# Performance work log

Hardware: AMD Instinct MI355X
Metric: run time of the kernel (lower is better)

## Reference

```python
import jax, jax.numpy as jnp
import numpy as np

BN_EPS = 1e-5


def setup_inputs() -> dict:
    key = jax.random.key(0)
    k1, k2, k3, k4 = jax.random.split(key, 4)
    B, H, W, C = 2, 256, 256, 256
    x = jax.random.normal(k1, (B, H, W, C), dtype=jnp.float32)
    # 1x1 conv weights (bias=False), randomly initialized each forward in the original
    w_down = jax.random.normal(k2, (16, C), dtype=jnp.float32) * (1.0 / np.sqrt(C))
    w_up = jax.random.normal(k3, (C, 16), dtype=jnp.float32) * (1.0 / np.sqrt(16))
    w_final = jax.random.normal(k4, (C, 2 * C), dtype=jnp.float32) * (1.0 / np.sqrt(2 * C))
    return {"x": x, "w_down": w_down, "w_up": w_up, "w_final": w_final}


def reference(x, w_down, w_up, w_final):
    # x: [B, H, W, C] -> NCHW
    x = jnp.transpose(x, (0, 3, 1, 2))  # [B, C, H, W]
    B, C, H, W = x.shape
    # fresh BatchNorm2d in training mode: batch stats, weight=1, bias=0
    mean = jnp.mean(x, axis=(0, 2, 3), keepdims=True)
    var = jnp.var(x, axis=(0, 2, 3), keepdims=True)  # biased variance
    xn = (x - mean) * jax.lax.rsqrt(var + BN_EPS)  # [B, C, H, W]
    # relu -> sigmoid
    a = jax.nn.sigmoid(jax.nn.relu(xn))
    # down-channel 1x1 conv: C -> 16
    y = jnp.einsum('oc,bchw->bohw', w_down, a)  # [B, 16, H, W]
    f = y.reshape(B, 16, H * W)  # flattened per-sample [16, HW]
    # channel self-attention; NOTE: source bug reuses Gram of sample 0 for sample 1
    G0 = f[0] @ f[0].T  # [16, 16]
    out0 = G0 @ f[0]    # [16, HW]
    out1 = G0 @ f[1]    # [16, HW]  (faithful to xcam4b = Dot(xcam3a, xcam1b))
    xcam4 = jnp.stack([out0, out1], axis=0).reshape(B, 16, H, W)
    # up-channel 1x1 conv: 16 -> C
    up = jnp.einsum('co,bohw->bchw', w_up, xcam4)  # [B, C, H, W]
    cat = jnp.concatenate([xn, up], axis=1)  # [B, 2C, H, W]
    # final down-channel 1x1 conv: 2C -> C
    out = jnp.einsum('oc,bchw->bohw', w_final, cat)  # [B, C, H, W]
    return out
```

## Files before the change

### kernel.cpp

```cpp
#include <hip/hip_runtime.h>
#include <hip/hip_bf16.h>
#include <stdint.h>

typedef __attribute__((ext_vector_type(8))) short bf16x8;
typedef __attribute__((ext_vector_type(4))) float f32x4;

#define CC 256
#define HWP 65536

__device__ __forceinline__ unsigned short f2bf(float f) {
    union { float f; unsigned int u; } v; v.f = f;
    unsigned int u = v.u;
    return (unsigned short)((u + 0x7fffu + ((u >> 16) & 1u)) >> 16);
}
__device__ __forceinline__ unsigned int pk2(float lo, float hi) {
    union { __hip_bfloat16 b; unsigned short s; } ul, uh;
    ul.b = __float2bfloat16(lo);
    uh.b = __float2bfloat16(hi);
    return (unsigned)ul.s | ((unsigned)uh.s << 16);
}
__device__ __forceinline__ float sigm_relu(float xn) {
    float xr = fmaxf(xn, 0.f);
    float e = __expf(-xr);
    return __builtin_amdgcn_rcpf(1.f + e);
}

__global__ __launch_bounds__(512, 8) void k1_part(const float* __restrict__ x,
                                                  float* __restrict__ part) {
    __shared__ float red[8][520];
    const int t = threadIdx.x, bid = blockIdx.x;
    const int c4 = (t & 63) * 4, po = t >> 6;
    const float* xp = x + ((size_t)(bid * 256 + po)) * CC + c4;
    f32x4 s = {0.f, 0.f, 0.f, 0.f}, q = {0.f, 0.f, 0.f, 0.f};
    #pragma unroll 8
    for (int p = 0; p < 32; ++p) {
        f32x4 v = *(const f32x4*)(xp + (size_t)p * 8 * CC);
        s += v; q += v * v;
    }
    *(f32x4*)&red[po][c4] = s;
    *(f32x4*)&red[po][256 + c4] = q;
    __syncthreads();
    float r = 0.f;
    #pragma unroll
    for (int po2 = 0; po2 < 8; ++po2) r += red[po2][t];
    part[bid * 512 + t] = r;
}

__global__ __launch_bounds__(256) void k2a_red(const float* __restrict__ part,
                                               float* __restrict__ p2) {
    int t = threadIdx.x, r = blockIdx.x;
    float s = 0.f, q = 0.f;
    #pragma unroll
    for (int i = 0; i < 16; ++i) {
        s += part[(size_t)(r * 16 + i) * 512 + t];
        q += part[(size_t)(r * 16 + i) * 512 + 256 + t];
    }
    p2[r * 512 + t] = s;
    p2[r * 512 + 256 + t] = q;
}

__global__ __launch_bounds__(256) void k2b_stats(const float* __restrict__ p2,
                                                 float* __restrict__ mg,
                                                 float* __restrict__ ig) {
    int c = threadIdx.x;
    float s = 0.f, q = 0.f;
    #pragma unroll
    for (int r = 0; r < 32; ++r) { s += p2[r * 512 + c]; q += p2[r * 512 + 256 + c]; }
    float mean = s * (1.f / 131072.f);
    float var  = q * (1.f / 131072.f) - mean * mean;
    mg[c] = mean;
    ig[c] = rsqrtf(var + 1e-5f);
}

__global__ __launch_bounds__(512) void k3_gram(const float* __restrict__ x,
                                               const float* __restrict__ wd,
                                               const float* __restrict__ mg,
                                               const float* __restrict__ ig,
                                               float* __restrict__ gpart) {
    __shared__ uint4 apack[2048];
    __shared__ float y_s[2][16][68];
    const int t = threadIdx.x;
    const int w = t >> 6, lm = t & 15, lk = (t >> 4) & 3;
    const int h = w & 1, ntile = w >> 1;
    uint4 wfrag[4];
    #pragma unroll
    for (int kt = 0; kt < 4; ++kt) {
        const int kbr = h * 16 + kt * 4 + lk;
        f32x4 wa = *(const f32x4*)(wd + lm * 256 + kbr * 8);
        f32x4 wb = *(const f32x4*)(wd + lm * 256 + kbr * 8 + 4);
        wfrag[kt] = (uint4){pk2(wa[0], wa[1]), pk2(wa[2], wa[3]),
                            pk2(wb[0], wb[1]), pk2(wb[2], wb[3])};
    }
    const int kb = t & 31, c0 = kb * 8, nb = t >> 5;
    f32x4 m0 = *(const f32x4*)(mg + c0), m1 = *(const f32x4*)(mg + c0 + 4);
    f32x4 i0 = *(const f32x4*)(ig + c0), i1 = *(const f32x4*)(ig + c0 + 4);
    const float mm[8] = {m0[0],m0[1],m0[2],m0[3],m1[0],m1[1],m1[2],m1[3]};
    const float ii[8] = {i0[0],i0[1],i0[2],i0[3],i1[0],i1[1],i1[2],i1[3]};
    const int o1 = t >> 4, o2 = t & 15;
    float g = 0.f;
    for (int st = 0; st < 4; ++st) {
        const float* xb = x + ((size_t)(blockIdx.x * 256 + st * 64 + nb)) * CC + c0;
        #pragma unroll
        for (int rep = 0; rep < 4; ++rep) {
            int n = rep * 16 + nb;
            const float* xp = xb + (size_t)rep * 16 * CC;
            f32x4 v0 = *(const f32x4*)xp;
            f32x4 v1 = *(const f32x4*)(xp + 4);
            float vv[8] = {v0[0],v0[1],v0[2],v0[3],v1[0],v1[1],v1[2],v1[3]};
            unsigned aw[4];
            #pragma unroll
            for (int hh = 0; hh < 4; ++hh) {
                float a0 = sigm_relu((vv[2*hh]   - mm[2*hh])   * ii[2*hh]);
                float a1 = sigm_relu((vv[2*hh+1] - mm[2*hh+1]) * ii[2*hh+1]);
                aw[hh] = pk2(a0, a1);
            }
            apack[kb * 64 + (n ^ kb)] = (uint4){aw[0], aw[1], aw[2], aw[3]};
        }
        __syncthreads();
        f32x4 accY = {0.f, 0.f, 0.f, 0.f};
        #pragma unroll
        for (int kt = 0; kt < 4; ++kt) {
            const int kbr = h * 16 + kt * 4 + lk;
            uint4 u = apack[kbr * 64 + ((ntile * 16 + lm) ^ kbr)];
            accY = __builtin_amdgcn_mfma_f32_16x16x32_bf16(*(bf16x8*)&wfrag[kt], *(bf16x8*)&u, accY, 0, 0, 0);
        }
        #pragma unroll
        for (int i = 0; i < 4; ++i) y_s[h][lk * 4 + i][ntile * 16 + lm] = accY[i];
        __syncthreads();
        if (t < 256) {
            #pragma unroll
            for (int p4 = 0; p4 < 16; ++p4) {
                f32x4 a0 = *(const f32x4*)&y_s[0][o1][p4 * 4];
                f32x4 a1 = *(const f32x4*)&y_s[1][o1][p4 * 4];
                f32x4 b0 = *(const f32x4*)&y_s[0][o2][p4 * 4];
                f32x4 b1 = *(const f32x4*)&y_s[1][o2][p4 * 4];
                f32x4 ya = a0 + a1, yb = b0 + b1;
                g += ya[0]*yb[0] + ya[1]*yb[1] + ya[2]*yb[2] + ya[3]*yb[3];
            }
        }
        __syncthreads();
    }
    if (t < 256) gpart[blockIdx.x * 256 + t] = g;
}

__global__ __launch_bounds__(256) void k45_wcb(const float* __restrict__ gpart,
                                               const float* __restrict__ wd,
                                               const float* __restrict__ wf,
                                               const float* __restrict__ wu,
                                               unsigned short* __restrict__ wcb) {
    __shared__ float G_s[256];
    __shared__ float R_s[16][256];
    __shared__ float M_s[16][17];
    const int t = threadIdx.x;
    float g = 0.f;
    #pragma unroll 8
    for (int i = 0; i < 256; ++i) g += gpart[i * 256 + t];
    G_s[t] = g;
    __syncthreads();
    #pragma unroll
    for (int o = 0; o < 16; ++o) {
        float r = 0.f;
        #pragma unroll
        for (int o2 = 0; o2 < 16; ++o2) r += G_s[o * 16 + o2] * wd[o2 * 256 + t];
        R_s[o][t] = r;
    }
    const int lr = t >> 4, j = t & 15;
    const int r = blockIdx.x * 16 + lr;
    const float* wfr = wf + (size_t)r * 512;
    float m = 0.f;
    for (int c = 0; c < 256; ++c) m += wfr[256 + c] * wu[c * 16 + j];
    M_s[lr][j] = m;
    __syncthreads();
    float Ml[16];
    #pragma unroll
    for (int o = 0; o < 16; ++o) Ml[o] = M_s[lr][o];
    unsigned short* wrow = wcb + (size_t)r * 512;
    for (int i = 0; i < 16; ++i) {
        int c = j + 16 * i;
        wrow[c] = f2bf(wfr[c]);
        float kv = 0.f;
        #pragma unroll
        for (int o = 0; o < 16; ++o) kv += Ml[o] * R_s[o][c];
        wrow[256 + c] = f2bf(kv);
    }
}

__global__ __launch_bounds__(512, 4) void k6_main(const float* __restrict__ x,
                                                  const unsigned short* __restrict__ wcb,
                                                  const float* __restrict__ mg,
                                                  const float* __restrict__ ig,
                                                  float* __restrict__ out) {
    __shared__ uint4 zpack[4096];
    const int t = threadIdx.x;
    const int tile = (blockIdx.x & 7) * 256 + (blockIdx.x >> 3);
    const int b = tile >> 10;
    const int pw = (tile & 1023) * 64;
    const int kb = t & 31, c0 = kb * 8, nb = t >> 5;
    f32x4 m0 = *(const f32x4*)(mg + c0), m1 = *(const f32x4*)(mg + c0 + 4);
    f32x4 i0 = *(const f32x4*)(ig + c0), i1 = *(const f32x4*)(ig + c0 + 4);
    const float mm[8] = {m0[0],m0[1],m0[2],m0[3],m1[0],m1[1],m1[2],m1[3]};
    const float ii[8] = {i0[0],i0[1],i0[2],i0[3],i1[0],i1[1],i1[2],i1[3]};
    const float* xb = x + ((size_t)(b * HWP + pw + nb)) * CC + c0;
    f32x4 v[8];
    #pragma unroll
    for (int rep = 0; rep < 4; ++rep) {
        v[2 * rep]     = *(const f32x4*)(xb + (size_t)rep * 16 * CC);
        v[2 * rep + 1] = *(const f32x4*)(xb + (size_t)rep * 16 * CC + 4);
    }
    #pragma unroll
    for (int rep = 0; rep < 4; ++rep) {
        const int px = rep * 16 + nb;
        f32x4 v0 = v[2 * rep], v1 = v[2 * rep + 1];
        float vv[8] = {v0[0],v0[1],v0[2],v0[3],v1[0],v1[1],v1[2],v1[3]};
        unsigned xw[4], aw[4];
        #pragma unroll
        for (int hh = 0; hh < 4; ++hh) {
            float xn0 = (vv[2*hh]   - mm[2*hh])   * ii[2*hh];
            float xn1 = (vv[2*hh+1] - mm[2*hh+1]) * ii[2*hh+1];
            xw[hh] = pk2(xn0, xn1);
            aw[hh] = pk2(sigm_relu(xn0), sigm_relu(xn1));
        }
        zpack[kb * 64 + ((px ^ kb) & 63)] = (uint4){xw[0], xw[1], xw[2], xw[3]};
        zpack[(kb + 32) * 64 + ((px ^ (kb + 32)) & 63)] = (uint4){aw[0], aw[1], aw[2], aw[3]};
    }
    __syncthreads();
    const int w = t >> 6, lm = t & 15, lk = (t >> 4) & 3;
    const unsigned short* wrow = wcb + (size_t)(w * 32 + lm) * 512 + lk * 8;
    f32x4 acc[4][2];
    #pragma unroll
    for (int mt = 0; mt < 4; ++mt)
        #pragma unroll
        for (int nt = 0; nt < 2; ++nt) acc[mt][nt] = (f32x4){0.f, 0.f, 0.f, 0.f};
    #pragma unroll 4
    for (int kt = 0; kt < 16; ++kt) {
        const int kbr = kt * 4 + lk;
        bf16x8 zfr[4], wfr[2];
        #pragma unroll
        for (int mt = 0; mt < 4; ++mt) {
            uint4 u = zpack[kbr * 64 + (((mt * 16 + lm) ^ kbr) & 63)];
            zfr[mt] = *(bf16x8*)&u;
        }
        #pragma unroll
        for (int nt = 0; nt < 2; ++nt)
            wfr[nt] = *(const bf16x8*)(wrow + (size_t)nt * 16 * 512 + kt * 32);
        #pragma unroll
        for (int mt = 0; mt < 4; ++mt)
            #pragma unroll
            for (int nt = 0; nt < 2; ++nt)
                acc[mt][nt] = __builtin_amdgcn_mfma_f32_16x16x32_bf16(zfr[mt], wfr[nt], acc[mt][nt], 0, 0, 0);
    }
    #pragma unroll
    for (int nt = 0; nt < 2; ++nt) {
        float* ob = out + ((size_t)(b * 256 + w * 32 + nt * 16 + lm)) * HWP + pw + lk * 4;
        #pragma unroll
        for (int mt = 0; mt < 4; ++mt)
            __builtin_nontemporal_store(acc[mt][nt], (f32x4*)(ob + mt * 16));
    }
}

extern "C" void kernel_launch(void* const* d_in, const int* in_sizes, int n_in,
                              void* d_out, int out_size, void* d_ws, size_t ws_size,
                              hipStream_t stream) {
    const float* x  = (const float*)d_in[0];
    const float* wd = (const float*)d_in[1];
    const float* wu = (const float*)d_in[2];
    const float* wf = (const float*)d_in[3];
    float* out = (float*)d_out;
    char* ws = (char*)d_ws;
    unsigned short* wcb = (unsigned short*)ws;
    float* part  = (float*)(ws + 262144);
    float* p2    = (float*)(ws + 1310720);
    float* mg    = (float*)(ws + 1376256);
    float* ig    = (float*)(ws + 1377280);
    float* gpart = (float*)(ws + 1378304);

    k1_part <<<dim3(512),  dim3(512), 0, stream>>>(x, part);
    k2a_red <<<dim3(32),   dim3(256), 0, stream>>>(part, p2);
    k2b_stats<<<dim3(1),   dim3(256), 0, stream>>>(p2, mg, ig);
    k3_gram <<<dim3(256),  dim3(512), 0, stream>>>(x, wd, mg, ig, gpart);
    k45_wcb <<<dim3(16),   dim3(256), 0, stream>>>(gpart, wd, wf, wu, wcb);
    k6_main <<<dim3(2048), dim3(512), 0, stream>>>(x, wcb, mg, ig, out);
}
```

Baseline: 150.7 us.

## Warp-specialize main GEMM kernel into producer and consumer waves with double-buffered LDS

The main kernel is split into four producer waves and four consumer waves. Producers load x, normalize it, apply the activation and write bf16 chunks into a double-buffered LDS tile. Consumers run MFMA over each K chunk while the producers fill the next one, and each consumer wave now computes a 64x64 output tile instead of 32x64. LDS use drops from 64KB to 32KB per block, which could allow more resident blocks. In exchange only half the waves issue MFMAs, the pipeline has only four stages separated by block-wide barriers, and the larger accumulators raise register pressure in the consumer waves.

```diff
diff --git a/kernel.cpp b/kernel.cpp
--- a/kernel.cpp
+++ b/kernel.cpp
@@ -190,72 +190,116 @@
                                                   const float* __restrict__ mg,
                                                   const float* __restrict__ ig,
                                                   float* __restrict__ out) {
-    __shared__ uint4 zpack[4096];
+    __shared__ uint4 zbuf[2][1024];
     const int t = threadIdx.x;
     const int tile = (blockIdx.x & 7) * 256 + (blockIdx.x >> 3);
     const int b = tile >> 10;
     const int pw = (tile & 1023) * 64;
-    const int kb = t & 31, c0 = kb * 8, nb = t >> 5;
-    f32x4 m0 = *(const f32x4*)(mg + c0), m1 = *(const f32x4*)(mg + c0 + 4);
-    f32x4 i0 = *(const f32x4*)(ig + c0), i1 = *(const f32x4*)(ig + c0 + 4);
-    const float mm[8] = {m0[0],m0[1],m0[2],m0[3],m1[0],m1[1],m1[2],m1[3]};
-    const float ii[8] = {i0[0],i0[1],i0[2],i0[3],i1[0],i1[1],i1[2],i1[3]};
-    const float* xb = x + ((size_t)(b * HWP + pw + nb)) * CC + c0;
-    f32x4 v[8];
-    #pragma unroll
-    for (int rep = 0; rep < 4; ++rep) {
-        v[2 * rep]     = *(const f32x4*)(xb + (size_t)rep * 16 * CC);
-        v[2 * rep + 1] = *(const f32x4*)(xb + (size_t)rep * 16 * CC + 4);
-    }
-    #pragma unroll
-    for (int rep = 0; rep < 4; ++rep) {
-        const int px = rep * 16 + nb;
-        f32x4 v0 = v[2 * rep], v1 = v[2 * rep + 1];
-        float vv[8] = {v0[0],v0[1],v0[2],v0[3],v1[0],v1[1],v1[2],v1[3]};
-        unsigned xw[4], aw[4];
-        #pragma unroll
-        for (int hh = 0; hh < 4; ++hh) {
-            float xn0 = (vv[2*hh]   - mm[2*hh])   * ii[2*hh];
-            float xn1 = (vv[2*hh+1] - mm[2*hh+1]) * ii[2*hh+1];
-            xw[hh] = pk2(xn0, xn1);
-            aw[hh] = pk2(sigm_relu(xn0), sigm_relu(xn1));
-        }
-        zpack[kb * 64 + ((px ^ kb) & 63)] = (uint4){xw[0], xw[1], xw[2], xw[3]};
-        zpack[(kb + 32) * 64 + ((px ^ (kb + 32)) & 63)] = (uint4){aw[0], aw[1], aw[2], aw[3]};
-    }
-    __syncthreads();
-    const int w = t >> 6, lm = t & 15, lk = (t >> 4) & 3;
-    const unsigned short* wrow = wcb + (size_t)(w * 32 + lm) * 512 + lk * 8;
-    f32x4 acc[4][2];
-    #pragma unroll
-    for (int mt = 0; mt < 4; ++mt)
-        #pragma unroll
-        for (int nt = 0; nt < 2; ++nt) acc[mt][nt] = (f32x4){0.f, 0.f, 0.f, 0.f};
-    #pragma unroll 4
-    for (int kt = 0; kt < 16; ++kt) {
-        const int kbr = kt * 4 + lk;
-        bf16x8 zfr[4], wfr[2];
-        #pragma unroll
-        for (int mt = 0; mt < 4; ++mt) {
-            uint4 u = zpack[kbr * 64 + (((mt * 16 + lm) ^ kbr) & 63)];
-            zfr[mt] = *(bf16x8*)&u;
-        }
-        #pragma unroll
-        for (int nt = 0; nt < 2; ++nt)
-            wfr[nt] = *(const bf16x8*)(wrow + (size_t)nt * 16 * 512 + kt * 32);
+    const int wv = t >> 6;
+    const bool prod = (wv < 4);
+    const int pk = t & 15, slot = (t >> 4) & 15;
+    const int w4 = wv & 3, lm = t & 15, lk = (t >> 4) & 3;
+
+    float mml[8], iil[8], mmh[8], iih[8];
+    f32x4 xv[8];
+    f32x4 acc[4][4];
+    const float* xb = x + ((size_t)(b * HWP + pw + slot)) * CC + pk * 8;
+
+#define LOADX(CB) do { \
+        _Pragma("unroll") \
+        for (int rep = 0; rep < 4; ++rep) { \
+            xv[2 * rep]     = *(const f32x4*)(xb + (size_t)rep * 16 * CC + (CB)); \
+            xv[2 * rep + 1] = *(const f32x4*)(xb + (size_t)rep * 16 * CC + (CB) + 4); \
+        } \
+    } while (0)
+
+#define STAGE(BUF, MMV, IIV, DO_A) do { \
+        _Pragma("unroll") \
+        for (int rep = 0; rep < 4; ++rep) { \
+            const int px = rep * 16 + slot; \
+            f32x4 v0 = xv[2 * rep], v1 = xv[2 * rep + 1]; \
+            float vv[8] = {v0[0],v0[1],v0[2],v0[3],v1[0],v1[1],v1[2],v1[3]}; \
+            unsigned zw[4]; \
+            _Pragma("unroll") \
+            for (int hh = 0; hh < 4; ++hh) { \
+                float xn0 = (vv[2*hh]   - (MMV)[2*hh])   * (IIV)[2*hh]; \
+                float xn1 = (vv[2*hh+1] - (MMV)[2*hh+1]) * (IIV)[2*hh+1]; \
+                if (DO_A) zw[hh] = pk2(sigm_relu(xn0), sigm_relu(xn1)); \
+                else      zw[hh] = pk2(xn0, xn1); \
+            } \
+            (BUF)[pk * 64 + ((px ^ pk) & 63)] = (uint4){zw[0], zw[1], zw[2], zw[3]}; \
+        } \
+    } while (0)
+
+#define CONSUME(BUF, KBASE) do { \
+        _Pragma("unroll") \
+        for (int ktc = 0; ktc < 4; ++ktc) { \
+            const int kbr = ktc * 4 + lk; \
+            bf16x8 zfr[4], wfr[4]; \
+            _Pragma("unroll") \
+            for (int pg = 0; pg < 4; ++pg) { \
+                uint4 u = (BUF)[kbr * 64 + (((pg * 16 + lm) ^ kbr) & 63)]; \
+                zfr[pg] = *(bf16x8*)&u; \
+            } \
+            _Pragma("unroll") \
+            for (int mt = 0; mt < 4; ++mt) \
+                wfr[mt] = *(const bf16x8*)(wcb + (size_t)(w4 * 64 + mt * 16 + lm) * 512 + (KBASE) + kbr * 8); \
+            _Pragma("unroll") \
+            for (int mt = 0; mt < 4; ++mt) \
+                _Pragma("unroll") \
+                for (int pg = 0; pg < 4; ++pg) \
+                    acc[mt][pg] = __builtin_amdgcn_mfma_f32_16x16x32_bf16(zfr[pg], wfr[mt], acc[mt][pg], 0, 0, 0); \
+        } \
+    } while (0)
+
+    if (prod) {
+        const int cl = pk * 8, ch = 128 + pk * 8;
+        f32x4 m0 = *(const f32x4*)(mg + cl), m1 = *(const f32x4*)(mg + cl + 4);
+        f32x4 i0 = *(const f32x4*)(ig + cl), i1 = *(const f32x4*)(ig + cl + 4);
+        f32x4 m2 = *(const f32x4*)(mg + ch), m3 = *(const f32x4*)(mg + ch + 4);
+        f32x4 i2 = *(const f32x4*)(ig + ch), i3 = *(const f32x4*)(ig + ch + 4);
+        #pragma unroll
+        for (int e = 0; e < 4; ++e) {
+            mml[e] = m0[e]; mml[4 + e] = m1[e];
+            iil[e] = i0[e]; iil[4 + e] = i1[e];
+            mmh[e] = m2[e]; mmh[4 + e] = m3[e];
+            iih[e] = i2[e]; iih[4 + e] = i3[e];
+        }
+        LOADX(0);
+        STAGE(zbuf[0], mml, iil, 0);
+    } else {
         #pragma unroll
         for (int mt = 0; mt < 4; ++mt)
             #pragma unroll
-            for (int nt = 0; nt < 2; ++nt)
-                acc[mt][nt] = __builtin_amdgcn_mfma_f32_16x16x32_bf16(zfr[mt], wfr[nt], acc[mt][nt], 0, 0, 0);
-    }
-    #pragma unroll
-    for (int nt = 0; nt < 2; ++nt) {
-        float* ob = out + ((size_t)(b * 256 + w * 32 + nt * 16 + lm)) * HWP + pw + lk * 4;
-        #pragma unroll
-        for (int mt = 0; mt < 4; ++mt)
-            __builtin_nontemporal_store(acc[mt][nt], (f32x4*)(ob + mt * 16));
-    }
+            for (int pg = 0; pg < 4; ++pg) acc[mt][pg] = (f32x4){0.f, 0.f, 0.f, 0.f};
+    }
+    __syncthreads();
+    if (prod) {
+        STAGE(zbuf[1], mml, iil, 1);
+        LOADX(128);
+    } else {
+        CONSUME(zbuf[0], 0);
+    }
+    __syncthreads();
+    if (prod) STAGE(zbuf[0], mmh, iih, 0);
+    else      CONSUME(zbuf[1], 256);
+    __syncthreads();
+    if (prod) STAGE(zbuf[1], mmh, iih, 1);
+    else      CONSUME(zbuf[0], 128);
+    __syncthreads();
+    if (!prod) {
+        CONSUME(zbuf[1], 384);
+        #pragma unroll
+        for (int mt = 0; mt < 4; ++mt) {
+            float* ob = out + ((size_t)(b * 256 + w4 * 64 + mt * 16 + lm)) * HWP + pw + lk * 4;
+            #pragma unroll
+            for (int pg = 0; pg < 4; ++pg)
+                __builtin_nontemporal_store(acc[mt][pg], (f32x4*)(ob + pg * 16));
+        }
+    }
+#undef LOADX
+#undef STAGE
+#undef CONSUME
 }
 
 extern "C" void kernel_launch(void* const* d_in, const int* in_sizes, int n_in,
```

Measured after the change: 247.5 us. +64.2%, slower.
